# Kernel tuning notes

Hardware: AMD Instinct MI355X
Metric: run time of the kernel (lower is better)

Reference implementation:

```python
import jax, jax.numpy as jnp
from jax import lax
import numpy as np

DIM = 384
HEADS = 8
MLP_HIDDEN = int(DIM * 4.0)
EPS = 1e-5


def layer_norm(x, g, b):
    m = jnp.mean(x, axis=-1, keepdims=True)
    v = jnp.mean((x - m) ** 2, axis=-1, keepdims=True)
    return (x - m) * lax.rsqrt(v + EPS) * g + b


def conv_pos_enc(x, H, W, w, b):
    # x: (B, N, C) -> depthwise 3x3 conv residual, act=Identity (cpe_act=False)
    B, N, C = x.shape
    feat = jnp.transpose(x, (0, 2, 1)).reshape(B, C, H, W)
    feat = lax.conv_general_dilated(
        feat, w, window_strides=(1, 1), padding='SAME',
        feature_group_count=C, dimension_numbers=('NCHW', 'OIHW', 'NCHW'))
    feat = feat + b[None, :, None, None]
    feat = jnp.transpose(feat.reshape(B, C, N), (0, 2, 1))
    return x + feat


def channel_attn(x, qkv_w, proj_w, proj_b):
    B, N, C = x.shape
    h = HEADS
    hd = C // h
    scale = hd ** (-0.5)
    qkv = x @ qkv_w.T                                # (B, N, 3C)
    qkv = qkv.reshape(B, N, 3, h, hd)
    qkv = jnp.transpose(qkv, (2, 0, 3, 1, 4))        # (3, B, h, N, hd)
    q, k, v = qkv[0], qkv[1], qkv[2]
    k = k * scale
    attn = jnp.einsum('bhnd,bhne->bhde', k, v)       # (B, h, hd, hd)
    attn = jax.nn.softmax(attn, axis=-1)
    out = jnp.einsum('bhde,bhne->bhnd', attn, q)     # (B, h, N, hd)
    out = jnp.transpose(out, (0, 2, 1, 3)).reshape(B, N, C)
    return out @ proj_w.T + proj_b


def mlp(x, fc1_w, fc1_b, fc2_w, fc2_b):
    h = jax.nn.gelu(x @ fc1_w.T + fc1_b, approximate=False)
    return h @ fc2_w.T + fc2_b


def setup_inputs() -> dict:
    key = jax.random.key(0)
    ks = jax.random.split(key, 12)
    C, Hd = DIM, MLP_HIDDEN
    s = 0.02
    return {
        'x': jax.random.normal(ks[0], (32, 784, C), dtype=jnp.float32),
        'H': 28,
        'W': 28,
        'cpe0_w': jax.random.normal(ks[1], (C, 1, 3, 3), dtype=jnp.float32) * s,
        'cpe0_b': jnp.zeros((C,), dtype=jnp.float32),
        'cpe1_w': jax.random.normal(ks[2], (C, 1, 3, 3), dtype=jnp.float32) * s,
        'cpe1_b': jnp.zeros((C,), dtype=jnp.float32),
        'norm1_g': jnp.ones((C,), dtype=jnp.float32),
        'norm1_b': jnp.zeros((C,), dtype=jnp.float32),
        'qkv_w': jax.random.normal(ks[3], (3 * C, C), dtype=jnp.float32) * s,
        'proj_w': jax.random.normal(ks[4], (C, C), dtype=jnp.float32) * s,
        'proj_b': jnp.zeros((C,), dtype=jnp.float32),
        'norm2_g': jnp.ones((C,), dtype=jnp.float32),
        'norm2_b': jnp.zeros((C,), dtype=jnp.float32),
        'fc1_w': jax.random.normal(ks[5], (Hd, C), dtype=jnp.float32) * s,
        'fc1_b': jnp.zeros((Hd,), dtype=jnp.float32),
        'fc2_w': jax.random.normal(ks[6], (C, Hd), dtype=jnp.float32) * s,
        'fc2_b': jnp.zeros((C,), dtype=jnp.float32),
    }


def reference(x, H, W, cpe0_w, cpe0_b, cpe1_w, cpe1_b, norm1_g, norm1_b,
              qkv_w, proj_w, proj_b, norm2_g, norm2_b,
              fc1_w, fc1_b, fc2_w, fc2_b):
    x = conv_pos_enc(x, H, W, cpe0_w, cpe0_b)
    cur = layer_norm(x, norm1_g, norm1_b)
    x = x + channel_attn(cur, qkv_w, proj_w, proj_b)
    x = conv_pos_enc(x, H, W, cpe1_w, cpe1_b)
    x = x + mlp(layer_norm(x, norm2_g, norm2_b), fc1_w, fc1_b, fc2_w, fc2_b)
    return x
```

## Files before the change

### kernel.cpp

```cpp
#include <hip/hip_runtime.h>
#include <hip/hip_bf16.h>
#include <math.h>
#include <stdint.h>

#define B_     32
#define HH_    28
#define WW_    28
#define N_     784
#define C_     384
#define M_     25088
#define HEADS_ 8
#define HD_    48
#define HID_   1536

typedef __bf16 bf16;
typedef __attribute__((ext_vector_type(8))) __bf16 bf16x8;
typedef __attribute__((ext_vector_type(4))) __bf16 bf16x4;
typedef __attribute__((ext_vector_type(4))) float f32x4;

__device__ __forceinline__ void gload_lds16(const void* g, void* l) {
    __builtin_amdgcn_global_load_lds(
        (const __attribute__((address_space(1))) unsigned int*)g,
        (__attribute__((address_space(3))) unsigned int*)(uintptr_t)l,
        16, 0, 0);
}

__global__ void convert4_kernel(const float* __restrict__ a, int na,
                                const float* __restrict__ b, int nb,
                                const float* __restrict__ c, int nc,
                                const float* __restrict__ d, int nd,
                                bf16* __restrict__ out) {
    int i = blockIdx.x * 256 + threadIdx.x;
    int j = i;
    const float* src;
    if (j < na) src = a + j;
    else { j -= na;
        if (j < nb) src = b + j;
        else { j -= nb;
            if (j < nc) src = c + j;
            else { j -= nc;
                if (j >= nd) return;
                src = d + j; } } }
    out[i] = (bf16)(*src);
}

__global__ __launch_bounds__(384)
void cpe_ln_kernel(const float* __restrict__ x, const float* __restrict__ w,
                   const float* __restrict__ bias, float* __restrict__ y,
                   const float* __restrict__ g, const float* __restrict__ beta,
                   bf16* __restrict__ lnout) {
    __shared__ float red[4][96];
    const int t = threadIdx.x;
    const int tpos = t / 96;
    const int cg = t - tpos * 96;
    const int c4 = cg * 4;
    const int row = blockIdx.x * 4 + tpos;
    const int b = row / N_;
    const int n = row - b * N_;
    const int py = n / WW_, px = n - py * WW_;
    const float* wc = w + c4 * 9;

    float4 acc = *(const float4*)(bias + c4);
    float4 ctr = *(const float4*)(x + (size_t)row * C_ + c4);

    if (py >= 1 && py <= 26 && px >= 1 && px <= 26) {
        const float* p0 = x + (size_t)(row - WW_ - 1) * C_ + c4;
        const float* p1 = p0 + (size_t)WW_ * C_;
        const float* p2 = p1 + (size_t)WW_ * C_;
        float4 a0 = *(const float4*)(p0);
        float4 a1 = *(const float4*)(p0 + C_);
        float4 a2 = *(const float4*)(p0 + 2 * C_);
        float4 b0 = *(const float4*)(p1);
        float4 b2 = *(const float4*)(p1 + 2 * C_);
        float4 c0 = *(const float4*)(p2);
        float4 c1 = *(const float4*)(p2 + C_);
        float4 c2 = *(const float4*)(p2 + 2 * C_);
        float4 b1 = ctr;
        #define TAP(V, TI) \
            acc.x += wc[TI] * V.x; acc.y += wc[9 + TI] * V.y; \
            acc.z += wc[18 + TI] * V.z; acc.w += wc[27 + TI] * V.w;
        TAP(a0, 0) TAP(a1, 1) TAP(a2, 2)
        TAP(b0, 3) TAP(b1, 4) TAP(b2, 5)
        TAP(c0, 6) TAP(c1, 7) TAP(c2, 8)
        #undef TAP
    } else {
        #pragma unroll
        for (int ky = 0; ky < 3; ky++) {
            int yy = py + ky - 1;
            if (yy < 0 || yy >= HH_) continue;
            #pragma unroll
            for (int kx = 0; kx < 3; kx++) {
                int xx = px + kx - 1;
                if (xx < 0 || xx >= WW_) continue;
                int tap = ky * 3 + kx;
                float4 xv = (ky == 1 && kx == 1) ? ctr
                          : *(const float4*)(x + (size_t)(b * N_ + yy * WW_ + xx) * C_ + c4);
                acc.x += wc[tap] * xv.x;
                acc.y += wc[9 + tap] * xv.y;
                acc.z += wc[18 + tap] * xv.z;
                acc.w += wc[27 + tap] * xv.w;
            }
        }
    }
    acc.x += ctr.x; acc.y += ctr.y; acc.z += ctr.z; acc.w += ctr.w;
    *(float4*)(y + (size_t)row * C_ + c4) = acc;

    red[tpos][cg] = acc.x + acc.y + acc.z + acc.w;
    __syncthreads();
    #pragma unroll
    for (int s = 48; s >= 3; s >>= 1) {
        if (cg < s) red[tpos][cg] += red[tpos][cg + s];
        __syncthreads();
    }
    float mean = (red[tpos][0] + red[tpos][1] + red[tpos][2]) * (1.f / C_);
    __syncthreads();
    float dx = acc.x - mean, dy = acc.y - mean, dz = acc.z - mean, dw = acc.w - mean;
    red[tpos][cg] = dx * dx + dy * dy + dz * dz + dw * dw;
    __syncthreads();
    #pragma unroll
    for (int s = 48; s >= 3; s >>= 1) {
        if (cg < s) red[tpos][cg] += red[tpos][cg + s];
        __syncthreads();
    }
    float var = (red[tpos][0] + red[tpos][1] + red[tpos][2]) * (1.f / C_);
    float rstd = rsqrtf(var + 1e-5f);
    float4 gv = *(const float4*)(g + c4);
    float4 bv = *(const float4*)(beta + c4);
    bf16x4 ov;
    ov[0] = (bf16)(dx * rstd * gv.x + bv.x);
    ov[1] = (bf16)(dy * rstd * gv.y + bv.y);
    ov[2] = (bf16)(dz * rstd * gv.z + bv.z);
    ov[3] = (bf16)(dw * rstd * gv.w + bv.w);
    *(bf16x4*)(lnout + (size_t)row * C_ + c4) = ov;
}

template<bool BIAS, bool GELU, bool RESID, bool OUTBF>
__global__ __launch_bounds__(256)
void gemm_kernel(const bf16* __restrict__ A, const bf16* __restrict__ Wt,
                 const float* __restrict__ bias, const float* __restrict__ resid,
                 void* __restrict__ outp, int M, int N, int K) {
    __shared__ __align__(16) bf16 As[3 * 4096];
    __shared__ __align__(16) bf16 Bs[3 * 4096];

    const int nbn = gridDim.x, nbm = gridDim.y;
    const int f = blockIdx.y * nbn + blockIdx.x;
    const int grp = f / (8 * nbn);
    const int rem = f - grp * 8 * nbn;
    const int rows = min(8, nbm - grp * 8);
    const int bm = (grp * 8 + rem % rows) * 128;
    const int bn = (rem / rows) * 128;

    const int t = threadIdx.x;
    const int wave = t >> 6, lane = t & 63;
    const int wm = (wave & 1) * 64, wn = (wave >> 1) * 64;
    const int quad = lane >> 4, r = lane & 15;

    const int ldrow = lane >> 2;
    const int ldcol = (lane & 3) * 8;
    const bf16* ga0 = A  + (size_t)(bm + wave * 32 + ldrow) * K + ldcol;
    const bf16* ga1 = ga0 + (size_t)16 * K;
    const bf16* gb0 = Wt + (size_t)(bn + wave * 32 + ldrow) * K + ldcol;
    const bf16* gb1 = gb0 + (size_t)16 * K;
    const int lbase = wave * 32 * 32;

    f32x4 acc[4][4] = {};

    gload_lds16(ga0, &As[lbase]);
    gload_lds16(ga1, &As[lbase + 512]);
    gload_lds16(gb0, &Bs[lbase]);
    gload_lds16(gb1, &Bs[lbase + 512]);
    gload_lds16(ga0 + 32, &As[4096 + lbase]);
    gload_lds16(ga1 + 32, &As[4096 + lbase + 512]);
    gload_lds16(gb0 + 32, &Bs[4096 + lbase]);
    gload_lds16(gb1 + 32, &Bs[4096 + lbase + 512]);

    int buf = 0;
    int k0 = 0;
    for (; k0 < K - 32; k0 += 32) {
        asm volatile("s_waitcnt vmcnt(4)" ::: "memory");
        asm volatile("s_barrier" ::: "memory");
        if (k0 + 64 < K) {
            const int nb3 = (buf == 0 ? 2 : buf - 1) * 4096;
            gload_lds16(ga0 + k0 + 64, &As[nb3 + lbase]);
            gload_lds16(ga1 + k0 + 64, &As[nb3 + lbase + 512]);
            gload_lds16(gb0 + k0 + 64, &Bs[nb3 + lbase]);
            gload_lds16(gb1 + k0 + 64, &Bs[nb3 + lbase + 512]);
        }
        const bf16* as = &As[buf * 4096];
        const bf16* bs = &Bs[buf * 4096];
        bf16x8 af[4], bfr[4];
        #pragma unroll
        for (int i = 0; i < 4; i++)
            af[i] = *(const bf16x8*)(&as[(wm + i * 16 + r) * 32 + quad * 8]);
        #pragma unroll
        for (int j = 0; j < 4; j++)
            bfr[j] = *(const bf16x8*)(&bs[(wn + j * 16 + r) * 32 + quad * 8]);
        #pragma unroll
        for (int i = 0; i < 4; i++)
            #pragma unroll
            for (int j = 0; j < 4; j++)
                acc[i][j] = __builtin_amdgcn_mfma_f32_16x16x32_bf16(af[i], bfr[j], acc[i][j], 0, 0, 0);
        buf = (buf == 2) ? 0 : buf + 1;
    }
    {
        asm volatile("s_waitcnt vmcnt(0)" ::: "memory");
        asm volatile("s_barrier" ::: "memory");
        const bf16* as = &As[buf * 4096];
        const bf16* bs = &Bs[buf * 4096];
        bf16x8 af[4], bfr[4];
        #pragma unroll
        for (int i = 0; i < 4; i++)
            af[i] = *(const bf16x8*)(&as[(wm + i * 16 + r) * 32 + quad * 8]);
        #pragma unroll
        for (int j = 0; j < 4; j++)
            bfr[j] = *(const bf16x8*)(&bs[(wn + j * 16 + r) * 32 + quad * 8]);
        #pragma unroll
        for (int i = 0; i < 4; i++)
            #pragma unroll
            for (int j = 0; j < 4; j++)
                acc[i][j] = __builtin_amdgcn_mfma_f32_16x16x32_bf16(af[i], bfr[j], acc[i][j], 0, 0, 0);
    }

    #pragma unroll
    for (int i = 0; i < 4; i++) {
        #pragma unroll
        for (int j = 0; j < 4; j++) {
            int n = bn + wn + j * 16 + r;
            float bv = BIAS ? bias[n] : 0.f;
            #pragma unroll
            for (int e = 0; e < 4; e++) {
                int m = bm + wm + i * 16 + quad * 4 + e;
                float val = acc[i][j][e] + bv;
                if (GELU) val = 0.5f * val * (1.f + erff(val * 0.70710678118654752f));
                if (RESID) val += resid[(size_t)m * N + n];
                if (OUTBF) ((bf16*)outp)[(size_t)m * N + n] = (bf16)val;
                else       ((float*)outp)[(size_t)m * N + n] = val;
            }
        }
    }
}

__global__ __launch_bounds__(256)
void attn_fused_kernel(const bf16* __restrict__ qkvb, bf16* __restrict__ outp) {
    __shared__ __align__(16) bf16 stage[4][3872];
    __shared__ float Sred[4][48][49];
    __shared__ __align__(16) bf16 attn_s[48 * 72];

    const int bh = blockIdx.x;
    const int b = bh >> 3, h = bh & 7;
    const int t = threadIdx.x;
    const int wave = t >> 6, lane = t & 63;
    const int quad = lane >> 4, r = lane & 15;
    const int tensor = lane >> 5;
    const int n_local = lane & 31;

    const size_t qkv_base = (size_t)b * N_ * 1152;
    const int toff = 384 + tensor * 384 + h * 48;

    f32x4 acc[3][3] = {};
    bf16* kT = &stage[wave][0];
    bf16* vT = &stage[wave][1936];
    bf16* myT = &stage[wave][tensor * 1936];

    for (int c = wave; c < 25; c += 4) {
        int n0 = c * 32;
        bf16 rowbuf[48];
        if (n0 + n_local < N_) {
            const uint4* src = (const uint4*)(qkvb + qkv_base + (size_t)(n0 + n_local) * 1152 + toff);
            #pragma unroll
            for (int i = 0; i < 6; i++) *(uint4*)(&rowbuf[i * 8]) = src[i];
        } else {
            #pragma unroll
            for (int i = 0; i < 48; i++) rowbuf[i] = (bf16)0.f;
        }
        #pragma unroll
        for (int d = 0; d < 48; d++) myT[d * 40 + n_local] = rowbuf[d];
        bf16x8 af[3], bfv[3];
        #pragma unroll
        for (int i = 0; i < 3; i++) af[i]  = *(const bf16x8*)(&kT[(i * 16 + r) * 40 + quad * 8]);
        #pragma unroll
        for (int j = 0; j < 3; j++) bfv[j] = *(const bf16x8*)(&vT[(j * 16 + r) * 40 + quad * 8]);
        #pragma unroll
        for (int i = 0; i < 3; i++)
            #pragma unroll
            for (int j = 0; j < 3; j++)
                acc[i][j] = __builtin_amdgcn_mfma_f32_16x16x32_bf16(af[i], bfv[j], acc[i][j], 0, 0, 0);
    }

    #pragma unroll
    for (int i = 0; i < 3; i++)
        #pragma unroll
        for (int j = 0; j < 3; j++)
            #pragma unroll
            for (int e = 0; e < 4; e++)
                Sred[wave][i * 16 + quad * 4 + e][j * 16 + r] = acc[i][j][e];
    __syncthreads();

    if (t < 48) {
        float row[48];
        float mx = -1e30f;
        #pragma unroll
        for (int e = 0; e < 48; e++) {
            float s = Sred[0][t][e] + Sred[1][t][e] + Sred[2][t][e] + Sred[3][t][e];
            s *= 0.14433756729740644f;
            row[e] = s;
            mx = fmaxf(mx, s);
        }
        float sum = 0.f;
        #pragma unroll
        for (int e = 0; e < 48; e++) { float ex = __expf(row[e] - mx); row[e] = ex; sum += ex; }
        float inv = 1.f / sum;
        #pragma unroll
        for (int e = 0; e < 48; e++) attn_s[t * 72 + e] = (bf16)(row[e] * inv);
        #pragma unroll
        for (int e = 48; e < 64; e++) attn_s[t * 72 + e] = (bf16)0.f;
    }
    __syncthreads();

    const bf16* qbase = qkvb + qkv_base + h * 48;
    for (int nt = wave; nt < 49; nt += 4) {
        int n0 = nt * 16;
        f32x4 oacc[3] = {};
        #pragma unroll
        for (int kc = 0; kc < 2; kc++) {
            bf16x8 bq = *(const bf16x8*)(qbase + (size_t)(n0 + r) * 1152 + kc * 32 + quad * 8);
            #pragma unroll
            for (int i = 0; i < 3; i++) {
                bf16x8 aa = *(const bf16x8*)(&attn_s[(i * 16 + r) * 72 + kc * 32 + quad * 8]);
                oacc[i] = __builtin_amdgcn_mfma_f32_16x16x32_bf16(aa, bq, oacc[i], 0, 0, 0);
            }
        }
        #pragma unroll
        for (int i = 0; i < 3; i++) {
            bf16x4 ov;
            #pragma unroll
            for (int e = 0; e < 4; e++) ov[e] = (bf16)oacc[i][e];
            *(bf16x4*)(outp + (size_t)(b * N_ + n0 + r) * 384 + h * 48 + i * 16 + quad * 4) = ov;
        }
    }
}

extern "C" void kernel_launch(void* const* d_in, const int* in_sizes, int n_in,
                              void* d_out, int out_size, void* d_ws, size_t ws_size,
                              hipStream_t stream) {
    const float* x      = (const float*)d_in[0];
    const float* cpe0_w = (const float*)d_in[3];
    const float* cpe0_b = (const float*)d_in[4];
    const float* cpe1_w = (const float*)d_in[5];
    const float* cpe1_b = (const float*)d_in[6];
    const float* n1g    = (const float*)d_in[7];
    const float* n1b    = (const float*)d_in[8];
    const float* qkv_w  = (const float*)d_in[9];
    const float* proj_w = (const float*)d_in[10];
    const float* proj_b = (const float*)d_in[11];
    const float* n2g    = (const float*)d_in[12];
    const float* n2b    = (const float*)d_in[13];
    const float* fc1_w  = (const float*)d_in[14];
    const float* fc1_b  = (const float*)d_in[15];
    const float* fc2_w  = (const float*)d_in[16];
    const float* fc2_b  = (const float*)d_in[17];

    char* ws = (char*)d_ws;
    size_t off = 0;
    bf16* cur    = (bf16*)(ws + off); off += (size_t)M_ * C_ * 2;
    bf16* qkvb   = (bf16*)(ws + off);
    float* x3    = (float*)qkvb;
    off += (size_t)M_ * 1152 * 2;
    bf16* hbuf   = (bf16*)(ws + off); off += (size_t)M_ * HID_ * 2;
    bf16* qkv_wb  = (bf16*)(ws + off); off += (size_t)1152 * 384 * 2;
    bf16* proj_wb = (bf16*)(ws + off); off += (size_t)384 * 384 * 2;
    bf16* fc1_wb  = (bf16*)(ws + off); off += (size_t)HID_ * 384 * 2;
    bf16* fc2_wb  = (bf16*)(ws + off); off += (size_t)384 * HID_ * 2;
    float* out = (float*)d_out;

    const int na = 442368, nb = 147456, nc = 589824, nd = 589824;
    convert4_kernel<<<(na + nb + nc + nd + 255) / 256, 256, 0, stream>>>(
        qkv_w, na, proj_w, nb, fc1_w, nc, fc2_w, nd, qkv_wb);

    cpe_ln_kernel<<<M_ / 4, 384, 0, stream>>>(x, cpe0_w, cpe0_b, out, n1g, n1b, cur);
    gemm_kernel<false, false, false, true><<<dim3(1152 / 128, M_ / 128), 256, 0, stream>>>(
        cur, qkv_wb, nullptr, nullptr, qkvb, M_, 1152, 384);
    attn_fused_kernel<<<256, 256, 0, stream>>>(qkvb, cur);
    gemm_kernel<true, false, true, false><<<dim3(384 / 128, M_ / 128), 256, 0, stream>>>(
        cur, proj_wb, proj_b, out, out, M_, 384, 384);
    cpe_ln_kernel<<<M_ / 4, 384, 0, stream>>>(out, cpe1_w, cpe1_b, x3, n2g, n2b, cur);
    gemm_kernel<true, true, false, true><<<dim3(HID_ / 128, M_ / 128), 256, 0, stream>>>(
        cur, fc1_wb, fc1_b, nullptr, hbuf, M_, HID_, 384);
    gemm_kernel<true, false, true, false><<<dim3(384 / 128, M_ / 128), 256, 0, stream>>>(
        hbuf, fc2_wb, fc2_b, x3, out, M_, 384, HID_);
}
```

Measured before the change: 419.9 us.

## Rewrite CPE+LayerNorm as wave-per-row with transposed conv weights and shuffle reductions

Measured after the change: 374.2 us. -10.9%, faster.

```diff
diff --git a/kernel.cpp b/kernel.cpp
--- a/kernel.cpp
+++ b/kernel.cpp
@@ -44,94 +44,89 @@
     out[i] = (bf16)(*src);
 }
 
-__global__ __launch_bounds__(384)
-void cpe_ln_kernel(const float* __restrict__ x, const float* __restrict__ w,
+__global__ void wtrans_kernel(const float* __restrict__ w0, const float* __restrict__ w1,
+                              float* __restrict__ wt0, float* __restrict__ wt1) {
+    int i = blockIdx.x * 256 + threadIdx.x;
+    if (i >= C_ * 9) return;
+    int c = i / 9, t = i - c * 9;
+    wt0[t * C_ + c] = w0[i];
+    wt1[t * C_ + c] = w1[i];
+}
+
+__global__ __launch_bounds__(256)
+void cpe_ln_kernel(const float* __restrict__ x, const float* __restrict__ wt,
                    const float* __restrict__ bias, float* __restrict__ y,
                    const float* __restrict__ g, const float* __restrict__ beta,
                    bf16* __restrict__ lnout) {
-    __shared__ float red[4][96];
-    const int t = threadIdx.x;
-    const int tpos = t / 96;
-    const int cg = t - tpos * 96;
-    const int c4 = cg * 4;
-    const int row = blockIdx.x * 4 + tpos;
+    const int wave = threadIdx.x >> 6, lane = threadIdx.x & 63;
+    const int f = blockIdx.x;
+    const int row = (f & 7) * 3136 + (f >> 3) * 4 + wave;
     const int b = row / N_;
     const int n = row - b * N_;
     const int py = n / WW_, px = n - py * WW_;
-    const float* wc = w + c4 * 9;
-
-    float4 acc = *(const float4*)(bias + c4);
-    float4 ctr = *(const float4*)(x + (size_t)row * C_ + c4);
+
+    float acc[6], ctr[6];
+    const float* xrow = x + (size_t)row * C_ + lane;
+    #pragma unroll
+    for (int j = 0; j < 6; j++) {
+        acc[j] = bias[lane + j * 64];
+        ctr[j] = xrow[j * 64];
+    }
 
     if (py >= 1 && py <= 26 && px >= 1 && px <= 26) {
-        const float* p0 = x + (size_t)(row - WW_ - 1) * C_ + c4;
-        const float* p1 = p0 + (size_t)WW_ * C_;
-        const float* p2 = p1 + (size_t)WW_ * C_;
-        float4 a0 = *(const float4*)(p0);
-        float4 a1 = *(const float4*)(p0 + C_);
-        float4 a2 = *(const float4*)(p0 + 2 * C_);
-        float4 b0 = *(const float4*)(p1);
-        float4 b2 = *(const float4*)(p1 + 2 * C_);
-        float4 c0 = *(const float4*)(p2);
-        float4 c1 = *(const float4*)(p2 + C_);
-        float4 c2 = *(const float4*)(p2 + 2 * C_);
-        float4 b1 = ctr;
-        #define TAP(V, TI) \
-            acc.x += wc[TI] * V.x; acc.y += wc[9 + TI] * V.y; \
-            acc.z += wc[18 + TI] * V.z; acc.w += wc[27 + TI] * V.w;
-        TAP(a0, 0) TAP(a1, 1) TAP(a2, 2)
-        TAP(b0, 3) TAP(b1, 4) TAP(b2, 5)
-        TAP(c0, 6) TAP(c1, 7) TAP(c2, 8)
-        #undef TAP
+        const float* p = x + (size_t)(row - WW_ - 1) * C_ + lane;
+        float v[9][6];
+        #pragma unroll
+        for (int t = 0; t < 9; t++) {
+            if (t == 4) continue;
+            const float* pt = p + ((t / 3) * WW_ + (t % 3)) * C_;
+            #pragma unroll
+            for (int j = 0; j < 6; j++) v[t][j] = pt[j * 64];
+        }
+        #pragma unroll
+        for (int t = 0; t < 9; t++) {
+            #pragma unroll
+            for (int j = 0; j < 6; j++) {
+                float xv = (t == 4) ? ctr[j] : v[t][j];
+                acc[j] += wt[t * C_ + lane + j * 64] * xv;
+            }
+        }
     } else {
         #pragma unroll
-        for (int ky = 0; ky < 3; ky++) {
-            int yy = py + ky - 1;
-            if (yy < 0 || yy >= HH_) continue;
-            #pragma unroll
-            for (int kx = 0; kx < 3; kx++) {
-                int xx = px + kx - 1;
-                if (xx < 0 || xx >= WW_) continue;
-                int tap = ky * 3 + kx;
-                float4 xv = (ky == 1 && kx == 1) ? ctr
-                          : *(const float4*)(x + (size_t)(b * N_ + yy * WW_ + xx) * C_ + c4);
-                acc.x += wc[tap] * xv.x;
-                acc.y += wc[9 + tap] * xv.y;
-                acc.z += wc[18 + tap] * xv.z;
-                acc.w += wc[27 + tap] * xv.w;
-            }
-        }
-    }
-    acc.x += ctr.x; acc.y += ctr.y; acc.z += ctr.z; acc.w += ctr.w;
-    *(float4*)(y + (size_t)row * C_ + c4) = acc;
-
-    red[tpos][cg] = acc.x + acc.y + acc.z + acc.w;
-    __syncthreads();
-    #pragma unroll
-    for (int s = 48; s >= 3; s >>= 1) {
-        if (cg < s) red[tpos][cg] += red[tpos][cg + s];
-        __syncthreads();
-    }
-    float mean = (red[tpos][0] + red[tpos][1] + red[tpos][2]) * (1.f / C_);
-    __syncthreads();
-    float dx = acc.x - mean, dy = acc.y - mean, dz = acc.z - mean, dw = acc.w - mean;
-    red[tpos][cg] = dx * dx + dy * dy + dz * dz + dw * dw;
-    __syncthreads();
-    #pragma unroll
-    for (int s = 48; s >= 3; s >>= 1) {
-        if (cg < s) red[tpos][cg] += red[tpos][cg + s];
-        __syncthreads();
-    }
-    float var = (red[tpos][0] + red[tpos][1] + red[tpos][2]) * (1.f / C_);
-    float rstd = rsqrtf(var + 1e-5f);
-    float4 gv = *(const float4*)(g + c4);
-    float4 bv = *(const float4*)(beta + c4);
-    bf16x4 ov;
-    ov[0] = (bf16)(dx * rstd * gv.x + bv.x);
-    ov[1] = (bf16)(dy * rstd * gv.y + bv.y);
-    ov[2] = (bf16)(dz * rstd * gv.z + bv.z);
-    ov[3] = (bf16)(dw * rstd * gv.w + bv.w);
-    *(bf16x4*)(lnout + (size_t)row * C_ + c4) = ov;
+        for (int t = 0; t < 9; t++) {
+            int yy = py + t / 3 - 1, xx = px + t % 3 - 1;
+            if (yy < 0 || yy >= HH_ || xx < 0 || xx >= WW_) continue;
+            const float* pt = x + (size_t)(b * N_ + yy * WW_ + xx) * C_ + lane;
+            #pragma unroll
+            for (int j = 0; j < 6; j++)
+                acc[j] += wt[t * C_ + lane + j * 64] * pt[j * 64];
+        }
+    }
+    #pragma unroll
+    for (int j = 0; j < 6; j++) acc[j] += ctr[j];
+
+    float* yrow = y + (size_t)row * C_ + lane;
+    #pragma unroll
+    for (int j = 0; j < 6; j++) yrow[j * 64] = acc[j];
+
+    float s = 0.f;
+    #pragma unroll
+    for (int j = 0; j < 6; j++) s += acc[j];
+    #pragma unroll
+    for (int off = 1; off < 64; off <<= 1) s += __shfl_xor(s, off, 64);
+    float mean = s * (1.f / C_);
+    float d[6], vs = 0.f;
+    #pragma unroll
+    for (int j = 0; j < 6; j++) { d[j] = acc[j] - mean; vs += d[j] * d[j]; }
+    #pragma unroll
+    for (int off = 1; off < 64; off <<= 1) vs += __shfl_xor(vs, off, 64);
+    float rstd = rsqrtf(vs * (1.f / C_) + 1e-5f);
+    bf16* lrow = lnout + (size_t)row * C_ + lane;
+    #pragma unroll
+    for (int j = 0; j < 6; j++) {
+        int c = lane + j * 64;
+        lrow[j * 64] = (bf16)(d[j] * rstd * g[c] + beta[c]);
+    }
 }
 
 template<bool BIAS, bool GELU, bool RESID, bool OUTBF>
@@ -371,19 +366,22 @@
     bf16* proj_wb = (bf16*)(ws + off); off += (size_t)384 * 384 * 2;
     bf16* fc1_wb  = (bf16*)(ws + off); off += (size_t)HID_ * 384 * 2;
     bf16* fc2_wb  = (bf16*)(ws + off); off += (size_t)384 * HID_ * 2;
+    float* wt0    = (float*)(ws + off); off += (size_t)C_ * 9 * 4;
+    float* wt1    = (float*)(ws + off); off += (size_t)C_ * 9 * 4;
     float* out = (float*)d_out;
 
     const int na = 442368, nb = 147456, nc = 589824, nd = 589824;
     convert4_kernel<<<(na + nb + nc + nd + 255) / 256, 256, 0, stream>>>(
         qkv_w, na, proj_w, nb, fc1_w, nc, fc2_w, nd, qkv_wb);
-
-    cpe_ln_kernel<<<M_ / 4, 384, 0, stream>>>(x, cpe0_w, cpe0_b, out, n1g, n1b, cur);
+    wtrans_kernel<<<(C_ * 9 + 255) / 256, 256, 0, stream>>>(cpe0_w, cpe1_w, wt0, wt1);
+
+    cpe_ln_kernel<<<M_ / 4, 256, 0, stream>>>(x, wt0, cpe0_b, out, n1g, n1b, cur);
     gemm_kernel<false, false, false, true><<<dim3(1152 / 128, M_ / 128), 256, 0, stream>>>(
         cur, qkv_wb, nullptr, nullptr, qkvb, M_, 1152, 384);
     attn_fused_kernel<<<256, 256, 0, stream>>>(qkvb, cur);
     gemm_kernel<true, false, true, false><<<dim3(384 / 128, M_ / 128), 256, 0, stream>>>(
         cur, proj_wb, proj_b, out, out, M_, 384, 384);
-    cpe_ln_kernel<<<M_ / 4, 384, 0, stream>>>(out, cpe1_w, cpe1_b, x3, n2g, n2b, cur);
+    cpe_ln_kernel<<<M_ / 4, 256, 0, stream>>>(out, wt1, cpe1_b, x3, n2g, n2b, cur);
     gemm_kernel<true, true, false, true><<<dim3(HID_ / 128, M_ / 128), 256, 0, stream>>>(
         cur, fc1_wb, fc1_b, nullptr, hbuf, M_, HID_, 384);
     gemm_kernel<true, false, true, false><<<dim3(384 / 128, M_ / 128), 256, 0, stream>>>(
```
